# Optimization experiments

Hardware: AMD Instinct MI355X
Metric: run time of the kernel (lower is better)

The kernel has to match this reference:

```python
import jax, jax.numpy as jnp
import numpy as np

N_NODES = 50000
N_EDGES = 400000
HID = 64
NUM_REL = 230
NUM_TS = 365
SLOPE = 0.2  # LeakyReLU negative slope

def lrelu(v):
    return jnp.where(v >= 0, v, SLOPE * v)

def setup_inputs() -> dict:
    key = jax.random.key(0)
    ks = jax.random.split(key, 10)
    x = jax.random.normal(ks[0], (N_NODES, 2 * HID), dtype=jnp.float32)
    rel_table = jax.random.normal(ks[1], (NUM_REL, HID), dtype=jnp.float32) * 0.1
    time_table = jax.random.normal(ks[2], (NUM_TS, HID), dtype=jnp.float32) * 0.1
    W_rt = jax.random.normal(ks[3], (2 * HID, 2 * HID), dtype=jnp.float32) * (1.0 / np.sqrt(2 * HID))
    b_rt = jnp.zeros((2 * HID,), dtype=jnp.float32)
    W_fc = jax.random.normal(ks[4], (6 * HID, 2 * HID), dtype=jnp.float32) * (1.0 / np.sqrt(6 * HID))
    b_fc = jnp.zeros((2 * HID,), dtype=jnp.float32)
    src = jax.random.randint(ks[5], (N_EDGES,), 0, N_NODES)
    dst = jax.random.randint(ks[6], (N_EDGES,), 0, N_NODES)
    rel = jax.random.randint(ks[7], (N_EDGES,), 0, NUM_REL)
    ts = jax.random.randint(ks[8], (N_EDGES,), 0, NUM_TS)
    edges = jnp.stack([src, dst, rel, ts], axis=1).astype(jnp.int64) if jax.config.jax_enable_x64 else jnp.stack([src, dst, rel, ts], axis=1)
    return {
        "x": x, "rel_table": rel_table, "time_table": time_table,
        "W_rt": W_rt, "b_rt": b_rt, "W_fc": W_fc, "b_fc": b_fc,
        "edges": edges, "num_nodes": N_NODES,
    }

def reference(x, rel_table, time_table, W_rt, b_rt, W_fc, b_fc, edges, num_nodes):
    # MessagePassing.forward + LogicalGNN.aggregated_messages (scatter_mean)
    src, dst, rel, ts = edges[:, 0], edges[:, 1], edges[:, 2], edges[:, 3]
    rel_e = rel_table[rel]          # [E, H]
    time_e = time_table[ts]         # [E, H]
    rel_t = lrelu(jnp.concatenate([rel_e, time_e], axis=-1) @ W_rt + b_rt)  # [E, 2H]
    msg_in = jnp.concatenate([x[src], rel_t, x[dst]], axis=-1)              # [E, 6H]
    messages = lrelu(msg_in @ W_fc + b_fc)                                  # [E, 2H]
    # scatter_mean over dst
    sums = jax.ops.segment_sum(messages, dst, num_segments=num_nodes)       # [N, 2H]
    counts = jax.ops.segment_sum(jnp.ones((messages.shape[0],), messages.dtype), dst, num_segments=num_nodes)
    agg = sums / jnp.maximum(counts, 1.0)[:, None]
    return agg
```

## Files before the change

### kernel.cpp

```cpp
#include <hip/hip_runtime.h>
#include <cstdio>

#define HID 64
#define D 128
#define NUM_REL 230
#define NUM_TS 365
#define NCOMB (NUM_REL*NUM_TS)
#define SLOPE 0.2f
#define XPAD 136
#define MAXDEG 64

typedef __attribute__((ext_vector_type(8))) short short8;
typedef __attribute__((ext_vector_type(4))) float f32x4;

__device__ __forceinline__ float lrelu(float v){ return v >= 0.f ? v : SLOPE*v; }

__device__ __forceinline__ unsigned bf_rne(float f){
    unsigned u = __float_as_uint(f);
    return (u + 0x7fffu + ((u >> 16) & 1u)) >> 16;
}
__device__ __forceinline__ unsigned pk2(float a, float b){
    return bf_rne(a) | (bf_rne(b) << 16);
}
__device__ __forceinline__ float bf_lo(unsigned u){ return __uint_as_float(u << 16); }
__device__ __forceinline__ float bf_hi(unsigned u){ return __uint_as_float(u & 0xffff0000u); }

__global__ __launch_bounds__(256) void k_scat(
        const int* __restrict__ edges, int n_edges,
        int* __restrict__ deg, int2* __restrict__ ebuf)
{
    int e0 = (blockIdx.x*256 + threadIdx.x)*4;
    const int4* ep = (const int4*)edges;
    if (e0 + 3 < n_edges) {
        int4 a = ep[e0+0];
        int4 b = ep[e0+1];
        int4 c = ep[e0+2];
        int4 d = ep[e0+3];
        int sa = atomicAdd(&deg[a.y], 1);
        int sb = atomicAdd(&deg[b.y], 1);
        int sc = atomicAdd(&deg[c.y], 1);
        int sd = atomicAdd(&deg[d.y], 1);
        if (sa < MAXDEG) ebuf[(size_t)a.y*MAXDEG + sa] = make_int2(a.x, a.z*NUM_TS + a.w);
        if (sb < MAXDEG) ebuf[(size_t)b.y*MAXDEG + sb] = make_int2(b.x, b.z*NUM_TS + b.w);
        if (sc < MAXDEG) ebuf[(size_t)c.y*MAXDEG + sc] = make_int2(c.x, c.z*NUM_TS + c.w);
        if (sd < MAXDEG) ebuf[(size_t)d.y*MAXDEG + sd] = make_int2(d.x, d.z*NUM_TS + d.w);
    } else {
        for (int e = e0; e < n_edges; ++e) {
            int4 ed = ep[e];
            int slot = atomicAdd(&deg[ed.y], 1);
            if (slot < MAXDEG)
                ebuf[(size_t)ed.y*MAXDEG + slot] = make_int2(ed.x, ed.z*NUM_TS + ed.w);
        }
    }
}

__global__ __launch_bounds__(256) void k_prep(
        const float* __restrict__ rel_table, const float* __restrict__ time_table,
        const float* __restrict__ W_rt, const float* __restrict__ W_fc,
        float* __restrict__ relP, float* __restrict__ timP,
        unsigned short* __restrict__ Wpk13, unsigned short* __restrict__ Wpk2)
{
    int b = blockIdx.x;
    if (b < 298) {
        int row = b*2 + (threadIdx.x >> 7);
        int j   = threadIdx.x & 127;
        if (row >= NUM_REL + NUM_TS) return;
        const float* tbl; const float* Wb; float* out;
        if (row < NUM_REL) { tbl = rel_table + row*HID;            Wb = W_rt;          out = relP + row*D; }
        else               { tbl = time_table + (row-NUM_REL)*HID; Wb = W_rt + HID*D;  out = timP + (row-NUM_REL)*D; }
        float acc = 0.f;
        #pragma unroll
        for (int k = 0; k < HID; ++k) acc += tbl[k] * Wb[k*D + j];
        out[j] = acc;
    } else {
        int id = (b - 298)*256 + threadIdx.x;
        if (id < 4096) {
            int mt = id >> 8;
            int s  = (id >> 6) & 3;
            int l  = id & 63;
            int m  = mt*16 + (l & 15);
            int kb = s*32 + (l >> 4)*8;
            unsigned short* dst = Wpk13 + ((size_t)(mt*4 + s)*64 + l)*8;
            #pragma unroll
            for (int j = 0; j < 8; ++j) {
                int k = kb + j;
                float v = (m < D) ? W_fc[(size_t)k*D + m]
                                  : W_fc[(size_t)(256 + k)*D + (m - D)];
                dst[j] = (unsigned short)bf_rne(v);
            }
        } else {
            int id2 = id - 4096;
            int mt = id2 >> 8;
            int s  = (id2 >> 6) & 3;
            int l  = id2 & 63;
            int m  = mt*16 + (l & 15);
            int kb = s*32 + (l >> 4)*8;
            unsigned short* dst = Wpk2 + ((size_t)(mt*4 + s)*64 + l)*8;
            #pragma unroll
            for (int j = 0; j < 8; ++j) {
                int k = kb + j;
                dst[j] = (unsigned short)bf_rne(W_fc[(size_t)(D + k)*D + m]);
            }
        }
    }
}

__device__ __forceinline__ void xw_body(
        int xb, const float* __restrict__ x,
        const unsigned short* __restrict__ Wpk13,
        unsigned short* __restrict__ xW13bf, int n_nodes,
        unsigned short* Xs )
{
    int t = threadIdx.x;
    int nodeBase = xb*64;
    {
        int row = t >> 2;
        int k0  = (t & 3)*32;
        int node = nodeBase + row;
        unsigned short* dst = Xs + row*XPAD + k0;
        if (node < n_nodes) {
            const float4* src = (const float4*)(x + (size_t)node*D + k0);
            #pragma unroll
            for (int g = 0; g < 8; ++g) {
                float4 v = src[g];
                *(uint2*)(dst + g*4) = make_uint2(pk2(v.x, v.y), pk2(v.z, v.w));
            }
        } else {
            #pragma unroll
            for (int g = 0; g < 8; ++g)
                *(uint2*)(dst + g*4) = make_uint2(0u, 0u);
        }
    }
    __syncthreads();

    int w = t >> 6, l = t & 63;
    int li = l & 15, q = l >> 4;

    f32x4 acc[4][4];
    #pragma unroll
    for (int mi = 0; mi < 4; ++mi)
        #pragma unroll
        for (int ni = 0; ni < 4; ++ni) acc[mi][ni] = (f32x4){0.f,0.f,0.f,0.f};

    #pragma unroll 1
    for (int s = 0; s < 4; ++s) {
        short8 af[4], bf[4];
        #pragma unroll
        for (int mi = 0; mi < 4; ++mi) {
            int mt = w*4 + mi;
            af[mi] = *(const short8*)(Wpk13 + ((size_t)(mt*4 + s)*64 + l)*8);
        }
        #pragma unroll
        for (int ni = 0; ni < 4; ++ni)
            bf[ni] = *(const short8*)(Xs + (ni*16 + li)*XPAD + s*32 + q*8);
        #pragma unroll
        for (int mi = 0; mi < 4; ++mi)
            #pragma unroll
            for (int ni = 0; ni < 4; ++ni)
                acc[mi][ni] = __builtin_amdgcn_mfma_f32_16x16x32_bf16(
                                  af[mi], bf[ni], acc[mi][ni], 0, 0, 0);
    }
    #pragma unroll
    for (int ni = 0; ni < 4; ++ni) {
        int node = nodeBase + ni*16 + li;
        if (node >= n_nodes) continue;
        #pragma unroll
        for (int mi = 0; mi < 4; ++mi) {
            int col = w*64 + mi*16 + q*4;
            *(uint2*)(xW13bf + (size_t)node*256 + col) =
                make_uint2(pk2(acc[mi][ni][0], acc[mi][ni][1]),
                           pk2(acc[mi][ni][2], acc[mi][ni][3]));
        }
    }
}

__device__ __forceinline__ void t2_body(
        int tb, const float* __restrict__ relP, const float* __restrict__ timP,
        const float* __restrict__ b_rt, const unsigned short* __restrict__ Wpk2,
        unsigned short* __restrict__ T2bf,
        unsigned short* Hs )
{
    int t = threadIdx.x;
    int cBase = tb*64;
    {
        int r  = t >> 2;
        int hk = (t & 3)*32;
        int combo = cBase + r;
        if (combo >= NCOMB) combo = NCOMB - 1;
        int rr = combo / NUM_TS;
        int tt = combo - rr*NUM_TS;
        const float4* rv4 = (const float4*)(relP + (size_t)rr*D + hk);
        const float4* tv4 = (const float4*)(timP + (size_t)tt*D + hk);
        const float4* bv4 = (const float4*)(b_rt + hk);
        unsigned short* dst = Hs + r*XPAD + hk;
        #pragma unroll
        for (int g = 0; g < 8; ++g) {
            float4 rv = rv4[g], tv = tv4[g], bv = bv4[g];
            float v0 = lrelu(rv.x+tv.x+bv.x), v1 = lrelu(rv.y+tv.y+bv.y);
            float v2 = lrelu(rv.z+tv.z+bv.z), v3 = lrelu(rv.w+tv.w+bv.w);
            *(uint2*)(dst + g*4) = make_uint2(pk2(v0,v1), pk2(v2,v3));
        }
    }
    __syncthreads();

    int w = t >> 6, l = t & 63;
    int li = l & 15, q = l >> 4;

    f32x4 acc[2][4];
    #pragma unroll
    for (int mi = 0; mi < 2; ++mi)
        #pragma unroll
        for (int ni = 0; ni < 4; ++ni) acc[mi][ni] = (f32x4){0.f,0.f,0.f,0.f};

    #pragma unroll 1
    for (int s = 0; s < 4; ++s) {
        short8 af[2], bf[4];
        #pragma unroll
        for (int mi = 0; mi < 2; ++mi) {
            int mt = w*2 + mi;
            af[mi] = *(const short8*)(Wpk2 + ((size_t)(mt*4 + s)*64 + l)*8);
        }
        #pragma unroll
        for (int ni = 0; ni < 4; ++ni)
            bf[ni] = *(const short8*)(Hs + (ni*16 + li)*XPAD + s*32 + q*8);
        #pragma unroll
        for (int mi = 0; mi < 2; ++mi)
            #pragma unroll
            for (int ni = 0; ni < 4; ++ni)
                acc[mi][ni] = __builtin_amdgcn_mfma_f32_16x16x32_bf16(
                                  af[mi], bf[ni], acc[mi][ni], 0, 0, 0);
    }
    #pragma unroll
    for (int ni = 0; ni < 4; ++ni) {
        int combo = cBase + ni*16 + li;
        if (combo >= NCOMB) continue;
        #pragma unroll
        for (int mi = 0; mi < 2; ++mi) {
            int col = (w*2 + mi)*16 + q*4;
            *(uint2*)(T2bf + (size_t)combo*D + col) =
                make_uint2(pk2(acc[mi][ni][0], acc[mi][ni][1]),
                           pk2(acc[mi][ni][2], acc[mi][ni][3]));
        }
    }
}

__global__ __launch_bounds__(256, 3) void k_mm(
        const float* __restrict__ x, const unsigned short* __restrict__ Wpk13,
        unsigned short* __restrict__ xW13bf, int n_nodes,
        const float* __restrict__ relP, const float* __restrict__ timP,
        const float* __restrict__ b_rt, const unsigned short* __restrict__ Wpk2,
        unsigned short* __restrict__ T2bf, int nxw)
{
    __shared__ __align__(16) unsigned short Hs[64*XPAD];
    int b = blockIdx.x;
    if (b < nxw) {
        xw_body(b, x, Wpk13, xW13bf, n_nodes, Hs);
    } else {
        t2_body(b - nxw, relP, timP, b_rt, Wpk2, T2bf, Hs);
    }
}

__global__ __launch_bounds__(256) void k_agg(
        const int* __restrict__ deg, const int2* __restrict__ ebuf,
        const unsigned short* __restrict__ xW13bf,
        const unsigned short* __restrict__ T2bf,
        const float* __restrict__ b_fc,
        float* __restrict__ out, int n_nodes)
{
    int t    = threadIdx.x;
    int lane = t & 63;
    int g    = lane >> 4;
    int sub  = lane & 15;
    int node = blockIdx.x*16 + (t >> 6)*4 + g;
    bool valid = node < n_nodes;
    int nodeC  = valid ? node : n_nodes - 1;

    int dg  = deg[nodeC];
    int cnt = valid ? (dg < MAXDEG ? dg : MAXDEG) : 0;
    int cm1 = cnt > 0 ? cnt - 1 : 0;
    const int2* eb = ebuf + (size_t)nodeC * MAXDEG;

    int cmax = cnt;
    cmax = max(cmax, __shfl_xor(cmax, 16));
    cmax = max(cmax, __shfl_xor(cmax, 32));

    float base[8];
    {
        uint4  w3  = *(const uint4*)&xW13bf[(size_t)nodeC*256 + 128 + sub*8];
        float4 blo = *(const float4*)&b_fc[sub*8];
        float4 bhi = *(const float4*)&b_fc[sub*8 + 4];
        base[0] = bf_lo(w3.x) + blo.x; base[1] = bf_hi(w3.x) + blo.y;
        base[2] = bf_lo(w3.y) + blo.z; base[3] = bf_hi(w3.y) + blo.w;
        base[4] = bf_lo(w3.z) + bhi.x; base[5] = bf_hi(w3.z) + bhi.y;
        base[6] = bf_lo(w3.w) + bhi.z; base[7] = bf_hi(w3.w) + bhi.w;
    }

    float acc[8];
    #pragma unroll
    for (int k = 0; k < 8; ++k) acc[k] = 0.f;

    const unsigned sMax = (unsigned)(n_nodes - 1);
    const unsigned cMax = (unsigned)(NCOMB - 1);

    for (int e = 0; e < cmax; e += 4) {
        int2 e0 = eb[min(e + 0, cm1)];
        int2 e1 = eb[min(e + 1, cm1)];
        int2 e2 = eb[min(e + 2, cm1)];
        int2 e3 = eb[min(e + 3, cm1)];
        unsigned s0 = min((unsigned)e0.x, sMax), c0 = min((unsigned)e0.y, cMax);
        unsigned s1 = min((unsigned)e1.x, sMax), c1 = min((unsigned)e1.y, cMax);
        unsigned s2 = min((unsigned)e2.x, sMax), c2 = min((unsigned)e2.y, cMax);
        unsigned s3 = min((unsigned)e3.x, sMax), c3 = min((unsigned)e3.y, cMax);
        uint4 S0 = *(const uint4*)&xW13bf[(size_t)s0*256 + sub*8];
        uint4 T0 = *(const uint4*)&T2bf  [(size_t)c0*D   + sub*8];
        uint4 S1 = *(const uint4*)&xW13bf[(size_t)s1*256 + sub*8];
        uint4 T1 = *(const uint4*)&T2bf  [(size_t)c1*D   + sub*8];
        uint4 S2 = *(const uint4*)&xW13bf[(size_t)s2*256 + sub*8];
        uint4 T2 = *(const uint4*)&T2bf  [(size_t)c2*D   + sub*8];
        uint4 S3 = *(const uint4*)&xW13bf[(size_t)s3*256 + sub*8];
        uint4 T3 = *(const uint4*)&T2bf  [(size_t)c3*D   + sub*8];
        bool m0 = (e + 0) < cnt, m1 = (e + 1) < cnt;
        bool m2 = (e + 2) < cnt, m3 = (e + 3) < cnt;
        #pragma unroll
        for (int w = 0; w < 4; ++w) {
            unsigned Sw0 = (&S0.x)[w], Tw0 = (&T0.x)[w];
            unsigned Sw1 = (&S1.x)[w], Tw1 = (&T1.x)[w];
            unsigned Sw2 = (&S2.x)[w], Tw2 = (&T2.x)[w];
            unsigned Sw3 = (&S3.x)[w], Tw3 = (&T3.x)[w];
            float v0l = lrelu(bf_lo(Sw0) + bf_lo(Tw0) + base[2*w]);
            float v0h = lrelu(bf_hi(Sw0) + bf_hi(Tw0) + base[2*w+1]);
            float v1l = lrelu(bf_lo(Sw1) + bf_lo(Tw1) + base[2*w]);
            float v1h = lrelu(bf_hi(Sw1) + bf_hi(Tw1) + base[2*w+1]);
            float v2l = lrelu(bf_lo(Sw2) + bf_lo(Tw2) + base[2*w]);
            float v2h = lrelu(bf_hi(Sw2) + bf_hi(Tw2) + base[2*w+1]);
            float v3l = lrelu(bf_lo(Sw3) + bf_lo(Tw3) + base[2*w]);
            float v3h = lrelu(bf_hi(Sw3) + bf_hi(Tw3) + base[2*w+1]);
            float a01l = (m0 ? v0l : 0.f) + (m1 ? v1l : 0.f);
            float a23l = (m2 ? v2l : 0.f) + (m3 ? v3l : 0.f);
            float a01h = (m0 ? v0h : 0.f) + (m1 ? v1h : 0.f);
            float a23h = (m2 ? v2h : 0.f) + (m3 ? v3h : 0.f);
            acc[2*w]   += a01l + a23l;
            acc[2*w+1] += a01h + a23h;
        }
    }

    if (!valid) return;
    float inv = 1.f / fmaxf((float)dg, 1.f);
    float4 o0 = make_float4(acc[0]*inv, acc[1]*inv, acc[2]*inv, acc[3]*inv);
    float4 o1 = make_float4(acc[4]*inv, acc[5]*inv, acc[6]*inv, acc[7]*inv);
    *(float4*)&out[(size_t)node*D + sub*8]     = o0;
    *(float4*)&out[(size_t)node*D + sub*8 + 4] = o1;
}

extern "C" void kernel_launch(void* const* d_in, const int* in_sizes, int n_in,
                              void* d_out, int out_size, void* d_ws, size_t ws_size,
                              hipStream_t stream)
{
    const float* x          = (const float*)d_in[0];
    const float* rel_table  = (const float*)d_in[1];
    const float* time_table = (const float*)d_in[2];
    const float* W_rt       = (const float*)d_in[3];
    const float* b_rt       = (const float*)d_in[4];
    const float* W_fc       = (const float*)d_in[5];
    const float* b_fc       = (const float*)d_in[6];
    const int*   edges      = (const int*)d_in[7];

    int n_nodes = in_sizes[0] / D;
    int n_edges = in_sizes[7] / 4;
    int nblkS   = (n_edges/4 + 255) / 256;
    int nxw     = (n_nodes + 63) / 64;
    int nt2     = (NCOMB + 63) / 64;

    char* ws = (char*)d_ws;
    size_t off = 0;
    auto alloc = [&](size_t bytes) -> void* {
        void* p = ws + off; off += (bytes + 255) & ~(size_t)255; return p;
    };
    unsigned short* xW13bf = (unsigned short*)alloc((size_t)n_nodes * 256 * 2);
    unsigned short* T2bf   = (unsigned short*)alloc((size_t)NCOMB * D * 2);
    unsigned short* Wpk13  = (unsigned short*)alloc((size_t)16*4*64*8 * 2);
    unsigned short* Wpk2   = (unsigned short*)alloc((size_t)8*4*64*8 * 2);
    float* relP   = (float*)alloc((size_t)NUM_REL * D * sizeof(float));
    float* timP   = (float*)alloc((size_t)NUM_TS * D * sizeof(float));
    int*   deg    = (int*)alloc((size_t)n_nodes * sizeof(int));
    int2*  ebuf   = (int2*)alloc((size_t)n_nodes * MAXDEG * sizeof(int2));
    if (off > ws_size)
        fprintf(stderr, "kernel_launch: workspace too small: need %zu, have %zu\n", off, ws_size);

    hipMemsetAsync(deg, 0, (size_t)n_nodes * sizeof(int), stream);

    k_scat<<<nblkS, 256, 0, stream>>>(edges, n_edges, deg, ebuf);
    k_prep<<<322, 256, 0, stream>>>(rel_table, time_table, W_rt, W_fc,
                                    relP, timP, Wpk13, Wpk2);
    k_mm  <<<nxw + nt2, 256, 0, stream>>>(x, Wpk13, xW13bf, n_nodes,
                                          relP, timP, b_rt, Wpk2, T2bf, nxw);
    k_agg <<<(n_nodes + 15)/16, 256, 0, stream>>>(deg, ebuf, xW13bf, T2bf,
                                                  b_fc, (float*)d_out, n_nodes);
}
```

Baseline: 187.3 us.

## Fuse edge scatter into matmul kernel with interleaved blocks and multi-tile persistence

Removes the separate k_scat launch and merges the edge-bucketing work into k_mm, interleaving scatter blocks evenly among the matmul blocks so atomic and memory-bound work overlaps with MFMA work. Each xW block now handles two 64-node tiles and each T2 block four 64-combo tiles, hoisting the weight fragments into registers once per block. This saves a launch and reloading of weights, at the cost of more registers, extra syncthreads per tile, and fewer blocks for load balancing.

```diff
diff --git a/kernel.cpp b/kernel.cpp
--- a/kernel.cpp
+++ b/kernel.cpp
@@ -24,35 +24,6 @@
 }
 __device__ __forceinline__ float bf_lo(unsigned u){ return __uint_as_float(u << 16); }
 __device__ __forceinline__ float bf_hi(unsigned u){ return __uint_as_float(u & 0xffff0000u); }
-
-__global__ __launch_bounds__(256) void k_scat(
-        const int* __restrict__ edges, int n_edges,
-        int* __restrict__ deg, int2* __restrict__ ebuf)
-{
-    int e0 = (blockIdx.x*256 + threadIdx.x)*4;
-    const int4* ep = (const int4*)edges;
-    if (e0 + 3 < n_edges) {
-        int4 a = ep[e0+0];
-        int4 b = ep[e0+1];
-        int4 c = ep[e0+2];
-        int4 d = ep[e0+3];
-        int sa = atomicAdd(&deg[a.y], 1);
-        int sb = atomicAdd(&deg[b.y], 1);
-        int sc = atomicAdd(&deg[c.y], 1);
-        int sd = atomicAdd(&deg[d.y], 1);
-        if (sa < MAXDEG) ebuf[(size_t)a.y*MAXDEG + sa] = make_int2(a.x, a.z*NUM_TS + a.w);
-        if (sb < MAXDEG) ebuf[(size_t)b.y*MAXDEG + sb] = make_int2(b.x, b.z*NUM_TS + b.w);
-        if (sc < MAXDEG) ebuf[(size_t)c.y*MAXDEG + sc] = make_int2(c.x, c.z*NUM_TS + c.w);
-        if (sd < MAXDEG) ebuf[(size_t)d.y*MAXDEG + sd] = make_int2(d.x, d.z*NUM_TS + d.w);
-    } else {
-        for (int e = e0; e < n_edges; ++e) {
-            int4 ed = ep[e];
-            int slot = atomicAdd(&deg[ed.y], 1);
-            if (slot < MAXDEG)
-                ebuf[(size_t)ed.y*MAXDEG + slot] = make_int2(ed.x, ed.z*NUM_TS + ed.w);
-        }
-    }
-}
 
 __global__ __launch_bounds__(256) void k_prep(
         const float* __restrict__ rel_table, const float* __restrict__ time_table,
@@ -105,141 +76,157 @@
     }
 }
 
-__device__ __forceinline__ void xw_body(
-        int xb, const float* __restrict__ x,
+__device__ __forceinline__ void xw_body2(
+        int xb2, const float* __restrict__ x,
         const unsigned short* __restrict__ Wpk13,
         unsigned short* __restrict__ xW13bf, int n_nodes,
         unsigned short* Xs )
 {
     int t = threadIdx.x;
-    int nodeBase = xb*64;
-    {
-        int row = t >> 2;
-        int k0  = (t & 3)*32;
-        int node = nodeBase + row;
-        unsigned short* dst = Xs + row*XPAD + k0;
-        if (node < n_nodes) {
-            const float4* src = (const float4*)(x + (size_t)node*D + k0);
-            #pragma unroll
-            for (int g = 0; g < 8; ++g) {
-                float4 v = src[g];
-                *(uint2*)(dst + g*4) = make_uint2(pk2(v.x, v.y), pk2(v.z, v.w));
-            }
-        } else {
-            #pragma unroll
-            for (int g = 0; g < 8; ++g)
-                *(uint2*)(dst + g*4) = make_uint2(0u, 0u);
-        }
-    }
-    __syncthreads();
-
     int w = t >> 6, l = t & 63;
     int li = l & 15, q = l >> 4;
 
-    f32x4 acc[4][4];
+    short8 af[4][4];
     #pragma unroll
-    for (int mi = 0; mi < 4; ++mi)
-        #pragma unroll
-        for (int ni = 0; ni < 4; ++ni) acc[mi][ni] = (f32x4){0.f,0.f,0.f,0.f};
+    for (int s = 0; s < 4; ++s)
+        #pragma unroll
+        for (int mi = 0; mi < 4; ++mi)
+            af[s][mi] = *(const short8*)(Wpk13 + ((size_t)((w*4 + mi)*4 + s)*64 + l)*8);
+
+    int row = t >> 2;
+    int k0  = (t & 3)*32;
 
     #pragma unroll 1
-    for (int s = 0; s < 4; ++s) {
-        short8 af[4], bf[4];
-        #pragma unroll
-        for (int mi = 0; mi < 4; ++mi) {
-            int mt = w*4 + mi;
-            af[mi] = *(const short8*)(Wpk13 + ((size_t)(mt*4 + s)*64 + l)*8);
-        }
-        #pragma unroll
-        for (int ni = 0; ni < 4; ++ni)
-            bf[ni] = *(const short8*)(Xs + (ni*16 + li)*XPAD + s*32 + q*8);
+    for (int r = 0; r < 2; ++r) {
+        int nodeBase = (xb2*2 + r)*64;
+        {
+            int node = nodeBase + row;
+            unsigned short* dst = Xs + row*XPAD + k0;
+            if (node < n_nodes) {
+                const float4* src = (const float4*)(x + (size_t)node*D + k0);
+                #pragma unroll
+                for (int g = 0; g < 8; ++g) {
+                    float4 v = src[g];
+                    *(uint2*)(dst + g*4) = make_uint2(pk2(v.x, v.y), pk2(v.z, v.w));
+                }
+            } else {
+                #pragma unroll
+                for (int g = 0; g < 8; ++g)
+                    *(uint2*)(dst + g*4) = make_uint2(0u, 0u);
+            }
+        }
+        __syncthreads();
+
+        f32x4 acc[4][4];
         #pragma unroll
         for (int mi = 0; mi < 4; ++mi)
             #pragma unroll
+            for (int ni = 0; ni < 4; ++ni) acc[mi][ni] = (f32x4){0.f,0.f,0.f,0.f};
+
+        #pragma unroll
+        for (int s = 0; s < 4; ++s) {
+            short8 bf[4];
+            #pragma unroll
             for (int ni = 0; ni < 4; ++ni)
-                acc[mi][ni] = __builtin_amdgcn_mfma_f32_16x16x32_bf16(
-                                  af[mi], bf[ni], acc[mi][ni], 0, 0, 0);
-    }
-    #pragma unroll
-    for (int ni = 0; ni < 4; ++ni) {
-        int node = nodeBase + ni*16 + li;
-        if (node >= n_nodes) continue;
-        #pragma unroll
-        for (int mi = 0; mi < 4; ++mi) {
-            int col = w*64 + mi*16 + q*4;
-            *(uint2*)(xW13bf + (size_t)node*256 + col) =
-                make_uint2(pk2(acc[mi][ni][0], acc[mi][ni][1]),
-                           pk2(acc[mi][ni][2], acc[mi][ni][3]));
-        }
-    }
-}
-
-__device__ __forceinline__ void t2_body(
-        int tb, const float* __restrict__ relP, const float* __restrict__ timP,
+                bf[ni] = *(const short8*)(Xs + (ni*16 + li)*XPAD + s*32 + q*8);
+            #pragma unroll
+            for (int mi = 0; mi < 4; ++mi)
+                #pragma unroll
+                for (int ni = 0; ni < 4; ++ni)
+                    acc[mi][ni] = __builtin_amdgcn_mfma_f32_16x16x32_bf16(
+                                      af[s][mi], bf[ni], acc[mi][ni], 0, 0, 0);
+        }
+        __syncthreads();
+
+        #pragma unroll
+        for (int ni = 0; ni < 4; ++ni) {
+            int node = nodeBase + ni*16 + li;
+            if (node >= n_nodes) continue;
+            #pragma unroll
+            for (int mi = 0; mi < 4; ++mi) {
+                int col = w*64 + mi*16 + q*4;
+                *(uint2*)(xW13bf + (size_t)node*256 + col) =
+                    make_uint2(pk2(acc[mi][ni][0], acc[mi][ni][1]),
+                               pk2(acc[mi][ni][2], acc[mi][ni][3]));
+            }
+        }
+    }
+}
+
+__device__ __forceinline__ void t2_body4(
+        int tb4, const float* __restrict__ relP, const float* __restrict__ timP,
         const float* __restrict__ b_rt, const unsigned short* __restrict__ Wpk2,
         unsigned short* __restrict__ T2bf,
         unsigned short* Hs )
 {
     int t = threadIdx.x;
-    int cBase = tb*64;
-    {
-        int r  = t >> 2;
-        int hk = (t & 3)*32;
-        int combo = cBase + r;
-        if (combo >= NCOMB) combo = NCOMB - 1;
-        int rr = combo / NUM_TS;
-        int tt = combo - rr*NUM_TS;
-        const float4* rv4 = (const float4*)(relP + (size_t)rr*D + hk);
-        const float4* tv4 = (const float4*)(timP + (size_t)tt*D + hk);
-        const float4* bv4 = (const float4*)(b_rt + hk);
-        unsigned short* dst = Hs + r*XPAD + hk;
-        #pragma unroll
-        for (int g = 0; g < 8; ++g) {
-            float4 rv = rv4[g], tv = tv4[g], bv = bv4[g];
-            float v0 = lrelu(rv.x+tv.x+bv.x), v1 = lrelu(rv.y+tv.y+bv.y);
-            float v2 = lrelu(rv.z+tv.z+bv.z), v3 = lrelu(rv.w+tv.w+bv.w);
-            *(uint2*)(dst + g*4) = make_uint2(pk2(v0,v1), pk2(v2,v3));
-        }
-    }
-    __syncthreads();
-
     int w = t >> 6, l = t & 63;
     int li = l & 15, q = l >> 4;
 
-    f32x4 acc[2][4];
+    short8 af[4][2];
     #pragma unroll
-    for (int mi = 0; mi < 2; ++mi)
-        #pragma unroll
-        for (int ni = 0; ni < 4; ++ni) acc[mi][ni] = (f32x4){0.f,0.f,0.f,0.f};
+    for (int s = 0; s < 4; ++s)
+        #pragma unroll
+        for (int mi = 0; mi < 2; ++mi)
+            af[s][mi] = *(const short8*)(Wpk2 + ((size_t)((w*2 + mi)*4 + s)*64 + l)*8);
+
+    int rrow = t >> 2;
+    int hk   = (t & 3)*32;
 
     #pragma unroll 1
-    for (int s = 0; s < 4; ++s) {
-        short8 af[2], bf[4];
-        #pragma unroll
-        for (int mi = 0; mi < 2; ++mi) {
-            int mt = w*2 + mi;
-            af[mi] = *(const short8*)(Wpk2 + ((size_t)(mt*4 + s)*64 + l)*8);
-        }
-        #pragma unroll
-        for (int ni = 0; ni < 4; ++ni)
-            bf[ni] = *(const short8*)(Hs + (ni*16 + li)*XPAD + s*32 + q*8);
+    for (int r = 0; r < 4; ++r) {
+        int cBase = (tb4*4 + r)*64;
+        {
+            int combo = cBase + rrow;
+            if (combo >= NCOMB) combo = NCOMB - 1;
+            int rr = combo / NUM_TS;
+            int tt = combo - rr*NUM_TS;
+            const float4* rv4 = (const float4*)(relP + (size_t)rr*D + hk);
+            const float4* tv4 = (const float4*)(timP + (size_t)tt*D + hk);
+            const float4* bv4 = (const float4*)(b_rt + hk);
+            unsigned short* dst = Hs + rrow*XPAD + hk;
+            #pragma unroll
+            for (int g = 0; g < 8; ++g) {
+                float4 rv = rv4[g], tv = tv4[g], bv = bv4[g];
+                float v0 = lrelu(rv.x+tv.x+bv.x), v1 = lrelu(rv.y+tv.y+bv.y);
+                float v2 = lrelu(rv.z+tv.z+bv.z), v3 = lrelu(rv.w+tv.w+bv.w);
+                *(uint2*)(dst + g*4) = make_uint2(pk2(v0,v1), pk2(v2,v3));
+            }
+        }
+        __syncthreads();
+
+        f32x4 acc[2][4];
         #pragma unroll
         for (int mi = 0; mi < 2; ++mi)
             #pragma unroll
+            for (int ni = 0; ni < 4; ++ni) acc[mi][ni] = (f32x4){0.f,0.f,0.f,0.f};
+
+        #pragma unroll
+        for (int s = 0; s < 4; ++s) {
+            short8 bf[4];
+            #pragma unroll
             for (int ni = 0; ni < 4; ++ni)
-                acc[mi][ni] = __builtin_amdgcn_mfma_f32_16x16x32_bf16(
-                                  af[mi], bf[ni], acc[mi][ni], 0, 0, 0);
-    }
-    #pragma unroll
-    for (int ni = 0; ni < 4; ++ni) {
-        int combo = cBase + ni*16 + li;
-        if (combo >= NCOMB) continue;
-        #pragma unroll
-        for (int mi = 0; mi < 2; ++mi) {
-            int col = (w*2 + mi)*16 + q*4;
-            *(uint2*)(T2bf + (size_t)combo*D + col) =
-                make_uint2(pk2(acc[mi][ni][0], acc[mi][ni][1]),
-                           pk2(acc[mi][ni][2], acc[mi][ni][3]));
+                bf[ni] = *(const short8*)(Hs + (ni*16 + li)*XPAD + s*32 + q*8);
+            #pragma unroll
+            for (int mi = 0; mi < 2; ++mi)
+                #pragma unroll
+                for (int ni = 0; ni < 4; ++ni)
+                    acc[mi][ni] = __builtin_amdgcn_mfma_f32_16x16x32_bf16(
+                                      af[s][mi], bf[ni], acc[mi][ni], 0, 0, 0);
+        }
+        __syncthreads();
+
+        #pragma unroll
+        for (int ni = 0; ni < 4; ++ni) {
+            int combo = cBase + ni*16 + li;
+            if (combo >= NCOMB) continue;
+            #pragma unroll
+            for (int mi = 0; mi < 2; ++mi) {
+                int col = (w*2 + mi)*16 + q*4;
+                *(uint2*)(T2bf + (size_t)combo*D + col) =
+                    make_uint2(pk2(acc[mi][ni][0], acc[mi][ni][1]),
+                               pk2(acc[mi][ni][2], acc[mi][ni][3]));
+            }
         }
     }
 }
@@ -249,14 +236,46 @@
         unsigned short* __restrict__ xW13bf, int n_nodes,
         const float* __restrict__ relP, const float* __restrict__ timP,
         const float* __restrict__ b_rt, const unsigned short* __restrict__ Wpk2,
-        unsigned short* __restrict__ T2bf, int nxw)
+        unsigned short* __restrict__ T2bf,
+        const int* __restrict__ edges, int n_edges,
+        int* __restrict__ deg, int2* __restrict__ ebuf,
+        int nsc, int nxwB, int ntot)
 {
     __shared__ __align__(16) unsigned short Hs[64*XPAD];
     int b = blockIdx.x;
-    if (b < nxw) {
-        xw_body(b, x, Wpk13, xW13bf, n_nodes, Hs);
+    int cumCur  = (int)(((long long)b       * nsc) / ntot);
+    int cumNext = (int)(((long long)(b + 1) * nsc) / ntot);
+    if (cumNext > cumCur) {
+        int e0 = (cumCur*256 + threadIdx.x)*4;
+        const int4* ep = (const int4*)edges;
+        if (e0 + 3 < n_edges) {
+            int4 a = ep[e0+0];
+            int4 bb = ep[e0+1];
+            int4 c = ep[e0+2];
+            int4 d = ep[e0+3];
+            int sa = atomicAdd(&deg[a.y], 1);
+            int sb = atomicAdd(&deg[bb.y], 1);
+            int sc = atomicAdd(&deg[c.y], 1);
+            int sd = atomicAdd(&deg[d.y], 1);
+            if (sa < MAXDEG) ebuf[(size_t)a.y*MAXDEG + sa] = make_int2(a.x, a.z*NUM_TS + a.w);
+            if (sb < MAXDEG) ebuf[(size_t)bb.y*MAXDEG + sb] = make_int2(bb.x, bb.z*NUM_TS + bb.w);
+            if (sc < MAXDEG) ebuf[(size_t)c.y*MAXDEG + sc] = make_int2(c.x, c.z*NUM_TS + c.w);
+            if (sd < MAXDEG) ebuf[(size_t)d.y*MAXDEG + sd] = make_int2(d.x, d.z*NUM_TS + d.w);
+        } else {
+            for (int e = e0; e < n_edges; ++e) {
+                int4 ed = ep[e];
+                int slot = atomicAdd(&deg[ed.y], 1);
+                if (slot < MAXDEG)
+                    ebuf[(size_t)ed.y*MAXDEG + slot] = make_int2(ed.x, ed.z*NUM_TS + ed.w);
+            }
+        }
     } else {
-        t2_body(b - nxw, relP, timP, b_rt, Wpk2, T2bf, Hs);
+        int cidx = b - cumNext;
+        if (cidx < nxwB) {
+            xw_body2(cidx, x, Wpk13, xW13bf, n_nodes, Hs);
+        } else {
+            t2_body4(cidx - nxwB, relP, timP, b_rt, Wpk2, T2bf, Hs);
+        }
     }
 }
 
@@ -367,9 +386,10 @@
 
     int n_nodes = in_sizes[0] / D;
     int n_edges = in_sizes[7] / 4;
-    int nblkS   = (n_edges/4 + 255) / 256;
-    int nxw     = (n_nodes + 63) / 64;
-    int nt2     = (NCOMB + 63) / 64;
+    int nsc     = (n_edges/4 + 255) / 256;
+    int nxwB    = ((n_nodes + 63)/64 + 1) / 2;
+    int nt2B    = ((NCOMB + 63)/64 + 3) / 4;
+    int ntot    = nsc + nxwB + nt2B;
 
     char* ws = (char*)d_ws;
     size_t off = 0;
@@ -389,11 +409,12 @@
 
     hipMemsetAsync(deg, 0, (size_t)n_nodes * sizeof(int), stream);
 
-    k_scat<<<nblkS, 256, 0, stream>>>(edges, n_edges, deg, ebuf);
     k_prep<<<322, 256, 0, stream>>>(rel_table, time_table, W_rt, W_fc,
                                     relP, timP, Wpk13, Wpk2);
-    k_mm  <<<nxw + nt2, 256, 0, stream>>>(x, Wpk13, xW13bf, n_nodes,
-                                          relP, timP, b_rt, Wpk2, T2bf, nxw);
+    k_mm  <<<ntot, 256, 0, stream>>>(x, Wpk13, xW13bf, n_nodes,
+                                     relP, timP, b_rt, Wpk2, T2bf,
+                                     edges, n_edges, deg, ebuf,
+                                     nsc, nxwB, ntot);
     k_agg <<<(n_nodes + 15)/16, 256, 0, stream>>>(deg, ebuf, xW13bf, T2bf,
                                                   b_fc, (float*)d_out, n_nodes);
 }
```

Result: no change. 187.9 us (+0.3%).
